# Kernel optimization log

Measured on AMD Instinct MI355X. Metric: run time of the kernel, lower is better.

The kernel has to match this reference:

```python
import jax, jax.numpy as jnp
import numpy as np

D = 768      # num_hiddens (hardcoded by dense1/dense2/ln in the source)
H = 12       # num_heads
NEG = -1000000.0
EPS = 1e-5


def setup_inputs() -> dict:
    key = jax.random.key(0)
    ks = jax.random.split(key, 14)
    B, Lq, Lk = 8, 1024, 1024
    s = 0.02
    return {
        "queries": jax.random.normal(ks[0], (B, Lq, D), dtype=jnp.float32),
        "keys":    jax.random.normal(ks[1], (B, Lk, D), dtype=jnp.float32),
        "values":  jax.random.normal(ks[2], (B, Lk, D), dtype=jnp.float32),
        # binary padding masks; count_nonzero along axis 1 gives valid lens
        "mask_1": jax.random.randint(ks[3], (B, Lk), 0, 2, dtype=jnp.int32),
        "mask_2": jax.random.randint(ks[4], (B, Lq), 0, 2, dtype=jnp.int32),
        # projection weights stored as [in, out] (torch Linear is y = x @ W.T)
        "Wq": jax.random.normal(ks[5], (D, D), dtype=jnp.float32) * s,
        "Wk": jax.random.normal(ks[6], (D, D), dtype=jnp.float32) * s,
        "Wv": jax.random.normal(ks[7], (D, D), dtype=jnp.float32) * s,
        "Wo": jax.random.normal(ks[8], (D, D), dtype=jnp.float32) * s,
        "d1_w": jax.random.normal(ks[9], (D, D), dtype=jnp.float32) * s,
        "d1_b": jnp.zeros((D,), dtype=jnp.float32),
        "d2_w": jax.random.normal(ks[10], (D, D), dtype=jnp.float32) * s,
        "d2_b": jnp.zeros((D,), dtype=jnp.float32),
        "ln_g": jnp.ones((D,), dtype=jnp.float32),
        "ln_b": jnp.zeros((D,), dtype=jnp.float32),
    }


def _cross_att(queries, keys, values, mask_1, mask_2,
               Wq, Wk, Wv, Wo, d1_w, d1_b, d2_w, d2_b, ln_g, ln_b):
    B, Lq, _ = queries.shape
    Lk = keys.shape[1]
    hd = D // H
    # project + split heads: [B, H, L, hd]
    q = (queries @ Wq).reshape(B, Lq, H, hd).transpose(0, 2, 1, 3)
    k = (keys    @ Wk).reshape(B, Lk, H, hd).transpose(0, 2, 1, 3)
    v = (values  @ Wv).reshape(B, Lk, H, hd).transpose(0, 2, 1, 3)
    scores = jnp.einsum('bhqd,bhkd->bhqk', q, k) / jnp.sqrt(jnp.float32(hd))
    # dual-axis prefix mask from nonzero counts
    vl1 = jnp.sum(mask_1 != 0, axis=1)  # [B], masks key axis
    vl2 = jnp.sum(mask_2 != 0, axis=1)  # [B], masks query axis
    col_ok = jnp.arange(Lk)[None, None, None, :] < vl1[:, None, None, None]
    row_ok = jnp.arange(Lq)[None, None, :, None] < vl2[:, None, None, None]
    scores = jnp.where(col_ok & row_ok, scores, NEG)
    attn = jax.nn.softmax(scores, axis=-1)
    out = jnp.einsum('bhqk,bhkd->bhqd', attn, v)
    out = out.transpose(0, 2, 1, 3).reshape(B, Lq, D)
    mha = out @ Wo
    ffn = jax.nn.relu(mha @ d1_w + d1_b) @ d2_w + d2_b
    x = ffn + mha  # dropout is identity in eval
    mu = jnp.mean(x, axis=-1, keepdims=True)
    var = jnp.mean(jnp.square(x - mu), axis=-1, keepdims=True)
    return (x - mu) / jnp.sqrt(var + EPS) * ln_g + ln_b


def reference(queries, keys, values, mask_1, mask_2,
              Wq, Wk, Wv, Wo, d1_w, d1_b, d2_w, d2_b, ln_g, ln_b):
    return _cross_att(queries, keys, values, mask_1, mask_2,
                      Wq, Wk, Wv, Wo, d1_w, d1_b, d2_w, d2_b, ln_g, ln_b)
```

## Files before the change

kernel.cpp:

```cpp
#include <hip/hip_runtime.h>
#include <hip/hip_bf16.h>
#include <type_traits>

#define DM   768
#define NH   12
#define HD   64
#define BATCH 8
#define SEQ  1024
#define NROWS (BATCH * SEQ)

typedef short bf16x8 __attribute__((ext_vector_type(8)));
typedef float f32x4 __attribute__((ext_vector_type(4)));

__device__ inline unsigned short f2b(float x) {
    union { float f; unsigned int u; } v; v.f = x;
    return (unsigned short)((v.u + 0x8000u) >> 16);
}
__device__ inline unsigned int f2b2(float lo, float hi) {
    union { float f; unsigned int u; } a, b; a.f = lo; b.f = hi;
    return __builtin_amdgcn_perm(b.u + 0x8000u, a.u + 0x8000u, 0x07060302u);
}
__device__ inline float b2f(unsigned short u) {
    union { float f; unsigned int x; } v; v.x = ((unsigned int)u) << 16;
    return v.f;
}

__device__ inline void gld16(const unsigned short* g, unsigned short* l) {
    __builtin_amdgcn_global_load_lds(
        (const __attribute__((address_space(1))) unsigned int*)g,
        (__attribute__((address_space(3))) unsigned int*)l, 16, 0, 0);
}

__global__ __launch_bounds__(256) void prep_kernel(const float* __restrict__ w0,
                                                   const float* __restrict__ w1,
                                                   const float* __restrict__ w2,
                                                   const float* __restrict__ w3,
                                                   const float* __restrict__ w4,
                                                   const float* __restrict__ w5,
                                                   unsigned short* __restrict__ wt,
                                                   const int* __restrict__ m1,
                                                   const int* __restrict__ m2,
                                                   int* __restrict__ lens,
                                                   const float* __restrict__ qin,
                                                   const float* __restrict__ kin,
                                                   const float* __restrict__ vin,
                                                   unsigned short* __restrict__ oq,
                                                   unsigned short* __restrict__ ok,
                                                   unsigned short* __restrict__ ov) {
    const int z = blockIdx.z;
    const int t = threadIdx.x;

    if (z >= 7) {
        const int linear = (z - 7) * 576 + blockIdx.y * 24 + blockIdx.x;
        const int g = linear / 3072;
        const int r = linear % 3072;
        const float* src = (g == 0) ? qin : (g == 1) ? kin : vin;
        unsigned short* dst = (g == 0) ? oq : (g == 1) ? ok : ov;
        const size_t i = ((size_t)r * 256 + t) * 8;
        float4 f0 = ((const float4*)(src + i))[0];
        float4 f1 = ((const float4*)(src + i))[1];
        uint4 p;
        p.x = f2b2(f0.x, f0.y); p.y = f2b2(f0.z, f0.w);
        p.z = f2b2(f1.x, f1.y); p.w = f2b2(f1.z, f1.w);
        *(uint4*)(dst + i) = p;
        return;
    }

    if (z < 6) {
        __shared__ float tile[32][33];
        const float* W = (z == 0) ? w0 : (z == 1) ? w1 : (z == 2) ? w2
                       : (z == 3) ? w3 : (z == 4) ? w4 : w5;
        unsigned short* Wt = wt + (size_t)z * DM * DM;
        const int n0 = blockIdx.x * 32;
        const int k0 = blockIdx.y * 32;
        const int tx = t & 31;
        const int ty = t >> 5;
#pragma unroll
        for (int r = 0; r < 4; ++r)
            tile[ty + 8 * r][tx] = W[(size_t)(k0 + ty + 8 * r) * DM + n0 + tx];
        __syncthreads();
#pragma unroll
        for (int r = 0; r < 4; ++r)
            Wt[(size_t)(n0 + ty + 8 * r) * DM + k0 + tx] = f2b(tile[tx][ty + 8 * r]);
        return;
    }

    if (blockIdx.y == 12) {
        if (blockIdx.x >= 16) return;
        __shared__ int redi[256];
        const int bid = blockIdx.x;
        const int b = bid & 7;
        const int* m = (bid < 8) ? m1 : m2;
        int cnt = 0;
        for (int i = t; i < SEQ; i += 256) cnt += (m[b * SEQ + i] != 0) ? 1 : 0;
        redi[t] = cnt;
        __syncthreads();
        for (int off = 128; off > 0; off >>= 1) {
            if (t < off) redi[t] += redi[t + off];
            __syncthreads();
        }
        if (t == 0) lens[bid] = redi[0];
        return;
    }

    if (blockIdx.x >= 12 || blockIdx.y >= 12) return;
    {
        __shared__ __align__(16) unsigned short As[64][40];
        __shared__ __align__(16) unsigned short Bs[64][40];
        unsigned short* out = wt + (size_t)6 * DM * DM;
        const float* Wo = w3;
        const float* d1w = w4;
        const int mb = blockIdx.x * 64;
        const int nb = blockIdx.y * 64;
        const int wid = t >> 6, lane = t & 63;
        const int quad = lane >> 4, l16 = lane & 15;
        const int bk = t >> 3, bn = (t & 7) * 8;
        const int am = t >> 2, ak = (t & 3) * 8;

        f32x4 acc[4];
#pragma unroll
        for (int c = 0; c < 4; ++c) acc[c] = (f32x4){0.f, 0.f, 0.f, 0.f};

        for (int j0 = 0; j0 < DM; j0 += 32) {
            {
                const float* s = &d1w[(size_t)(j0 + bk) * DM + mb + bn];
                float4 f0 = ((const float4*)s)[0];
                float4 f1 = ((const float4*)s)[1];
                As[bn + 0][bk] = f2b(f0.x); As[bn + 1][bk] = f2b(f0.y);
                As[bn + 2][bk] = f2b(f0.z); As[bn + 3][bk] = f2b(f0.w);
                As[bn + 4][bk] = f2b(f1.x); As[bn + 5][bk] = f2b(f1.y);
                As[bn + 6][bk] = f2b(f1.z); As[bn + 7][bk] = f2b(f1.w);
            }
            {
                const float* s = &Wo[(size_t)(nb + am) * DM + j0 + ak];
                float4 f0 = ((const float4*)s)[0];
                float4 f1 = ((const float4*)s)[1];
                uint4 p;
                p.x = f2b2(f0.x, f0.y); p.y = f2b2(f0.z, f0.w);
                p.z = f2b2(f1.x, f1.y); p.w = f2b2(f1.z, f1.w);
                *(uint4*)&Bs[am][ak] = p;
            }
            __syncthreads();
            bf16x8 av = *(const bf16x8*)&As[16 * wid + l16][quad * 8];
#pragma unroll
            for (int c = 0; c < 4; ++c) {
                bf16x8 bv = *(const bf16x8*)&Bs[16 * c + l16][quad * 8];
                acc[c] = __builtin_amdgcn_mfma_f32_16x16x32_bf16(av, bv, acc[c], 0, 0, 0);
            }
            __syncthreads();
        }
#pragma unroll
        for (int c = 0; c < 4; ++c) {
            const int col = nb + 16 * c + l16;
#pragma unroll
            for (int r = 0; r < 4; ++r) {
                const int row = mb + 16 * wid + quad * 4 + r;
                out[(size_t)row * DM + col] = f2b(acc[c][r]);
            }
        }
    }
}

__global__ __launch_bounds__(256) void qkv_gemm(const unsigned short* __restrict__ aq,
                                                const unsigned short* __restrict__ akk,
                                                const unsigned short* __restrict__ av_,
                                                const unsigned short* __restrict__ wt,
                                                unsigned short* __restrict__ c0,
                                                unsigned short* __restrict__ c1,
                                                unsigned short* __restrict__ c2) {
    __shared__ __align__(16) unsigned short As[128][32];
    __shared__ __align__(16) unsigned short Ws[128][32];

    const int t = threadIdx.x;
    const int g = blockIdx.y / 6;
    const int m0 = blockIdx.x * 128;
    const int n0 = (blockIdx.y % 6) * 128;
    const unsigned short* A = (g == 0) ? aq : (g == 1) ? akk : av_;
    const unsigned short* Wt = wt + (size_t)g * DM * DM;
    unsigned short* C = (g == 0) ? c0 : (g == 1) ? c1 : c2;
    const float cs = (g == 0) ? 0.18033688f : 1.0f;

    const int w = t >> 6, lane = t & 63;
    const int quad = lane >> 4, l16 = lane & 15;
    const int wm = w & 1, wn = w >> 1;
    const int srow = 16 * w + (lane >> 2);
    const int scol = 8 * ((lane & 3) ^ ((lane >> 3) & 3));
    const int swr = (quad ^ ((l16 >> 1) & 3)) * 8;

    f32x4 acc[4][4];
#pragma unroll
    for (int i = 0; i < 4; ++i)
#pragma unroll
        for (int j = 0; j < 4; ++j) acc[i][j] = (f32x4){0.f, 0.f, 0.f, 0.f};

    for (int k0 = 0; k0 < DM; k0 += 32) {
#pragma unroll
        for (int j = 0; j < 2; ++j) {
            gld16(&A[(size_t)(m0 + srow + 64 * j) * DM + k0 + scol],
                  &As[16 * w + 64 * j][0]);
            gld16(&Wt[(size_t)(n0 + srow + 64 * j) * DM + k0 + scol],
                  &Ws[16 * w + 64 * j][0]);
        }
        __syncthreads();

        bf16x8 av[4], bv[4];
#pragma unroll
        for (int i = 0; i < 4; ++i)
            av[i] = *(const bf16x8*)&As[wm * 64 + 16 * i + l16][swr];
#pragma unroll
        for (int i = 0; i < 4; ++i)
            bv[i] = *(const bf16x8*)&Ws[wn * 64 + 16 * i + l16][swr];
#pragma unroll
        for (int i = 0; i < 4; ++i)
#pragma unroll
            for (int j = 0; j < 4; ++j)
                acc[i][j] = __builtin_amdgcn_mfma_f32_16x16x32_bf16(av[i], bv[j], acc[i][j], 0, 0, 0);
        __syncthreads();
    }

#pragma unroll
    for (int i = 0; i < 4; ++i)
#pragma unroll
        for (int j = 0; j < 4; ++j) {
            const int gn = n0 + wn * 64 + 16 * j + l16;
#pragma unroll
            for (int r = 0; r < 4; ++r) {
                const int gm = m0 + wm * 64 + 16 * i + quad * 4 + r;
                C[(size_t)gm * DM + gn] = f2b(acc[i][j][r] * cs);
            }
        }
}

__global__ __launch_bounds__(256) void vpart_kernel(const unsigned short* __restrict__ v,
                                                    float* __restrict__ vp) {
    __shared__ float red[4][64];
    const int t = threadIdx.x;
    const int bh = blockIdx.x;
    const int chunk = blockIdx.y;
    const int b = bh / NH, h = bh % NH;
    const int d = t & 63, rg = t >> 6;
    const unsigned short* base =
        v + (size_t)(b * SEQ + chunk * 128 + rg * 32) * DM + h * HD + d;
    float s = 0.0f;
#pragma unroll 4
    for (int i = 0; i < 32; ++i) s += b2f(base[(size_t)i * DM]);
    red[rg][d] = s;
    __syncthreads();
    if (rg == 0)
        vp[((size_t)bh * 8 + chunk) * 64 + d] = red[0][d] + red[1][d] + red[2][d] + red[3][d];
}

template <typename CT>
__global__ __launch_bounds__(256) void gemm_bf(const unsigned short* __restrict__ A,
                                               const unsigned short* __restrict__ Wt,
                                               CT* __restrict__ C,
                                               const float* __restrict__ bias,
                                               const unsigned short* __restrict__ res,
                                               int relu) {
    __shared__ __align__(16) unsigned short As[128][32];
    __shared__ __align__(16) unsigned short Ws[128][32];

    const int t = threadIdx.x;
    const int m0 = blockIdx.x * 128;
    const int n0 = blockIdx.y * 128;
    const int w = t >> 6, lane = t & 63;
    const int quad = lane >> 4, l16 = lane & 15;
    const int wm = w & 1, wn = w >> 1;
    const int srow = 16 * w + (lane >> 2);
    const int scol = 8 * ((lane & 3) ^ ((lane >> 3) & 3));
    const int swr = (quad ^ ((l16 >> 1) & 3)) * 8;

    f32x4 acc[4][4];
#pragma unroll
    for (int i = 0; i < 4; ++i)
#pragma unroll
        for (int j = 0; j < 4; ++j) acc[i][j] = (f32x4){0.f, 0.f, 0.f, 0.f};

    for (int k0 = 0; k0 < DM; k0 += 32) {
#pragma unroll
        for (int j = 0; j < 2; ++j) {
            gld16(&A[(size_t)(m0 + srow + 64 * j) * DM + k0 + scol],
                  &As[16 * w + 64 * j][0]);
            gld16(&Wt[(size_t)(n0 + srow + 64 * j) * DM + k0 + scol],
                  &Ws[16 * w + 64 * j][0]);
        }
        __syncthreads();

        bf16x8 av[4], bv[4];
#pragma unroll
        for (int i = 0; i < 4; ++i)
            av[i] = *(const bf16x8*)&As[wm * 64 + 16 * i + l16][swr];
#pragma unroll
        for (int i = 0; i < 4; ++i)
            bv[i] = *(const bf16x8*)&Ws[wn * 64 + 16 * i + l16][swr];
#pragma unroll
        for (int i = 0; i < 4; ++i)
#pragma unroll
            for (int j = 0; j < 4; ++j)
                acc[i][j] = __builtin_amdgcn_mfma_f32_16x16x32_bf16(av[i], bv[j], acc[i][j], 0, 0, 0);
        __syncthreads();
    }

#pragma unroll
    for (int i = 0; i < 4; ++i)
#pragma unroll
        for (int j = 0; j < 4; ++j) {
            const int gn = n0 + wn * 64 + 16 * j + l16;
            const float badd = bias ? bias[gn] : 0.0f;
#pragma unroll
            for (int r = 0; r < 4; ++r) {
                const int gm = m0 + wm * 64 + 16 * i + quad * 4 + r;
                float cv = acc[i][j][r] + badd;
                if (relu) cv = fmaxf(cv, 0.0f);
                if (res) cv += b2f(res[(size_t)gm * DM + gn]);
                if constexpr (std::is_same<CT, float>::value) {
                    C[(size_t)gm * DM + gn] = cv;
                } else {
                    C[(size_t)gm * DM + gn] = f2b(cv);
                }
            }
        }
}

__global__ __launch_bounds__(256) void gemm_mh(const unsigned short* __restrict__ A,
                                               const unsigned short* __restrict__ wt,
                                               unsigned short* __restrict__ cm,
                                               unsigned short* __restrict__ ch,
                                               const float* __restrict__ d1b) {
    __shared__ __align__(16) unsigned short As[128][32];
    __shared__ __align__(16) unsigned short Ws[128][32];

    const int t = threadIdx.x;
    const int unit = blockIdx.y / 6;
    const unsigned short* Wt = wt + (size_t)(unit ? 6 : 3) * DM * DM;
    unsigned short* C = unit ? ch : cm;
    const int m0 = blockIdx.x * 128;
    const int n0 = (blockIdx.y % 6) * 128;
    const int w = t >> 6, lane = t & 63;
    const int quad = lane >> 4, l16 = lane & 15;
    const int wm = w & 1, wn = w >> 1;
    const int srow = 16 * w + (lane >> 2);
    const int scol = 8 * ((lane & 3) ^ ((lane >> 3) & 3));
    const int swr = (quad ^ ((l16 >> 1) & 3)) * 8;

    f32x4 acc[4][4];
#pragma unroll
    for (int i = 0; i < 4; ++i)
#pragma unroll
        for (int j = 0; j < 4; ++j) acc[i][j] = (f32x4){0.f, 0.f, 0.f, 0.f};

    for (int k0 = 0; k0 < DM; k0 += 32) {
#pragma unroll
        for (int j = 0; j < 2; ++j) {
            gld16(&A[(size_t)(m0 + srow + 64 * j) * DM + k0 + scol],
                  &As[16 * w + 64 * j][0]);
            gld16(&Wt[(size_t)(n0 + srow + 64 * j) * DM + k0 + scol],
                  &Ws[16 * w + 64 * j][0]);
        }
        __syncthreads();

        bf16x8 av[4], bv[4];
#pragma unroll
        for (int i = 0; i < 4; ++i)
            av[i] = *(const bf16x8*)&As[wm * 64 + 16 * i + l16][swr];
#pragma unroll
        for (int i = 0; i < 4; ++i)
            bv[i] = *(const bf16x8*)&Ws[wn * 64 + 16 * i + l16][swr];
#pragma unroll
        for (int i = 0; i < 4; ++i)
#pragma unroll
            for (int j = 0; j < 4; ++j)
                acc[i][j] = __builtin_amdgcn_mfma_f32_16x16x32_bf16(av[i], bv[j], acc[i][j], 0, 0, 0);
        __syncthreads();
    }

#pragma unroll
    for (int i = 0; i < 4; ++i)
#pragma unroll
        for (int j = 0; j < 4; ++j) {
            const int gn = n0 + wn * 64 + 16 * j + l16;
            const float badd = unit ? d1b[gn] : 0.0f;
#pragma unroll
            for (int r = 0; r < 4; ++r) {
                const int gm = m0 + wm * 64 + 16 * i + quad * 4 + r;
                float cv = acc[i][j][r] + badd;
                if (unit) cv = fmaxf(cv, 0.0f);
                C[(size_t)gm * DM + gn] = f2b(cv);
            }
        }
}

__global__ __launch_bounds__(256) void attn_mfma(const unsigned short* Q,
                                                 const unsigned short* __restrict__ K,
                                                 const unsigned short* __restrict__ V,
                                                 unsigned short* O,
                                                 const int* __restrict__ lens,
                                                 const float* __restrict__ vp) {
    __shared__ __align__(16) unsigned short Ks[64][72];
    __shared__ __align__(16) unsigned short Vt[64][72];
    __shared__ __align__(16) unsigned short Ps[4][16][72];

    const int t = threadIdx.x;
    const int bid = blockIdx.x;
    const int q0 = (bid & 15) * 64;
    const int h = (bid >> 4) % NH;
    const int b = bid / (16 * NH);
    const int vl1 = lens[b];
    const int vl2 = lens[8 + b];
    const int wid = t >> 6;
    const int lane = t & 63;
    const int quad = lane >> 4;
    const int l16 = lane & 15;
    const size_t vpb = (size_t)(b * NH + h) * 8 * 64;

    if (q0 >= vl2 || vl1 == 0) {
        float vm[4];
#pragma unroll
        for (int ct = 0; ct < 4; ++ct) {
            float s = 0.0f;
#pragma unroll
            for (int c = 0; c < 8; ++c) s += vp[vpb + (size_t)c * 64 + 16 * ct + l16];
            vm[ct] = s * (1.0f / 1024.0f);
        }
#pragma unroll
        for (int r = 0; r < 4; ++r) {
            const size_t row = (size_t)(b * SEQ + q0 + 16 * wid + quad * 4 + r);
#pragma unroll
            for (int ct = 0; ct < 4; ++ct)
                O[row * DM + h * HD + 16 * ct + l16] = f2b(vm[ct]);
        }
        return;
    }

    bf16x8 qa0, qa1;
    {
        const unsigned short* qp =
            &Q[(size_t)(b * SEQ + q0 + 16 * wid + l16) * DM + h * HD + quad * 8];
        qa0 = *(const bf16x8*)qp;
        qa1 = *(const bf16x8*)(qp + 32);
    }

    f32x4 o[4];
#pragma unroll
    for (int ct = 0; ct < 4; ++ct) o[ct] = (f32x4){0.f, 0.f, 0.f, 0.f};
    float suml[4];
    bool rbad[4];
#pragma unroll
    for (int r = 0; r < 4; ++r) {
        suml[r] = 0.0f;
        rbad[r] = (q0 + 16 * wid + quad * 4 + r) >= vl2;
    }

    const int nt = (vl1 + 63) >> 6;

    const int kkr = t >> 3;
    const int khc = (t & 7) * 8;
    const unsigned short* kbase = &K[(size_t)(b * SEQ) * DM + h * HD];
    const unsigned short* vbase = &V[(size_t)(b * SEQ) * DM + h * HD];

    uint4 kr0 = *(const uint4*)&kbase[(size_t)kkr * DM + khc];
    uint4 kr1 = *(const uint4*)&kbase[(size_t)(kkr + 32) * DM + khc];
    uint4 vr0 = *(const uint4*)&vbase[(size_t)lane * DM + wid * 16];
    uint4 vr1 = *(const uint4*)&vbase[(size_t)lane * DM + wid * 16 + 8];

    const int k2 = l16 >> 2;

    for (int tile = 0; tile < nt; ++tile) {
        const int c0 = tile * 64;
        *(uint4*)&Ks[kkr][khc] = kr0;
        *(uint4*)&Ks[kkr + 32][khc] = kr1;
        {
            union { uint4 u; unsigned short s[8]; } va, vb;
            va.u = vr0; vb.u = vr1;
#pragma unroll
            for (int j = 0; j < 8; ++j) Vt[wid * 16 + j][lane] = va.s[j];
#pragma unroll
            for (int j = 0; j < 8; ++j) Vt[wid * 16 + 8 + j][lane] = vb.s[j];
        }
        __syncthreads();

        if (tile < nt - 1) {
            const int c1 = c0 + 64;
            kr0 = *(const uint4*)&kbase[(size_t)(c1 + kkr) * DM + khc];
            kr1 = *(const uint4*)&kbase[(size_t)(c1 + kkr + 32) * DM + khc];
            vr0 = *(const uint4*)&vbase[(size_t)(c1 + lane) * DM + wid * 16];
            vr1 = *(const uint4*)&vbase[(size_t)(c1 + lane) * DM + wid * 16 + 8];
        }

        f32x4 s[4];
#pragma unroll
        for (int ct = 0; ct < 4; ++ct) {
            f32x4 acc = (f32x4){0.f, 0.f, 0.f, 0.f};
            bf16x8 b0v = *(const bf16x8*)&Ks[16 * ct + l16][quad * 8];
            bf16x8 b1v = *(const bf16x8*)&Ks[16 * ct + l16][32 + quad * 8];
            acc = __builtin_amdgcn_mfma_f32_16x16x32_bf16(qa0, b0v, acc, 0, 0, 0);
            acc = __builtin_amdgcn_mfma_f32_16x16x32_bf16(qa1, b1v, acc, 0, 0, 0);
            s[ct] = acc;
        }
#pragma unroll
        for (int ct = 0; ct < 4; ++ct) {
            const bool kok = (c0 + 16 * ct + l16) < vl1;
#pragma unroll
            for (int r = 0; r < 4; ++r) {
                float e = __builtin_amdgcn_exp2f(s[ct][r]);
                float p = kok ? e : 0.0f;
                s[ct][r] = p;
                suml[r] += p;
            }
        }
#pragma unroll
        for (int ct = 0; ct < 4; ++ct) {
            const int gidx = 2 * ct + (l16 >> 3);
            const int c = l16 & 7;
            const int gs = (gidx ^ quad) * 8 + c;
#pragma unroll
            for (int r = 0; r < 4; ++r)
                Ps[wid][quad * 4 + r][gs] = f2b(s[ct][r]);
        }
        bf16x8 pa0 = *(const bf16x8*)&Ps[wid][l16][(quad ^ k2) * 8];
        bf16x8 pa1 = *(const bf16x8*)&Ps[wid][l16][((4 + quad) ^ k2) * 8];
#pragma unroll
        for (int ct = 0; ct < 4; ++ct) {
            bf16x8 vb0 = *(const bf16x8*)&Vt[16 * ct + l16][quad * 8];
            bf16x8 vb1 = *(const bf16x8*)&Vt[16 * ct + l16][32 + quad * 8];
            o[ct] = __builtin_amdgcn_mfma_f32_16x16x32_bf16(pa0, vb0, o[ct], 0, 0, 0);
            o[ct] = __builtin_amdgcn_mfma_f32_16x16x32_bf16(pa1, vb1, o[ct], 0, 0, 0);
        }
        __syncthreads();
    }

#pragma unroll
    for (int d = 1; d < 16; d <<= 1) {
#pragma unroll
        for (int r = 0; r < 4; ++r) suml[r] += __shfl_xor(suml[r], d, 64);
    }

    float vm[4];
    if (rbad[0] || rbad[3]) {
#pragma unroll
        for (int ct = 0; ct < 4; ++ct) {
            float s = 0.0f;
#pragma unroll
            for (int c = 0; c < 8; ++c) s += vp[vpb + (size_t)c * 64 + 16 * ct + l16];
            vm[ct] = s * (1.0f / 1024.0f);
        }
    }
#pragma unroll
    for (int r = 0; r < 4; ++r) {
        const float inv = 1.0f / suml[r];
        const size_t row = (size_t)(b * SEQ + q0 + 16 * wid + quad * 4 + r);
#pragma unroll
        for (int ct = 0; ct < 4; ++ct) {
            const float val = rbad[r] ? vm[ct] : o[ct][r] * inv;
            O[row * DM + h * HD + 16 * ct + l16] = f2b(val);
        }
    }
}

__global__ __launch_bounds__(256) void ln_kernel(float* __restrict__ X,
                                                 const float* __restrict__ g,
                                                 const float* __restrict__ bvec) {
    __shared__ float red[256];
    const int row = blockIdx.x;
    const int t = threadIdx.x;
    float* xr = X + (size_t)row * DM;
    float x0 = xr[t];
    float x1 = xr[t + 256];
    float x2 = xr[t + 512];
    red[t] = x0 + x1 + x2;
    __syncthreads();
    for (int off = 128; off > 0; off >>= 1) {
        if (t < off) red[t] += red[t + off];
        __syncthreads();
    }
    float mu = red[0] * (1.0f / 768.0f);
    __syncthreads();
    float d0 = x0 - mu, d1 = x1 - mu, d2 = x2 - mu;
    red[t] = d0 * d0 + d1 * d1 + d2 * d2;
    __syncthreads();
    for (int off = 128; off > 0; off >>= 1) {
        if (t < off) red[t] += red[t + off];
        __syncthreads();
    }
    float rstd = rsqrtf(red[0] * (1.0f / 768.0f) + 1e-5f);
    xr[t]       = d0 * rstd * g[t]       + bvec[t];
    xr[t + 256] = d1 * rstd * g[t + 256] + bvec[t + 256];
    xr[t + 512] = d2 * rstd * g[t + 512] + bvec[t + 512];
}

extern "C" void kernel_launch(void* const* d_in, const int* in_sizes, int n_in,
                              void* d_out, int out_size, void* d_ws, size_t ws_size,
                              hipStream_t stream) {
    const float* queries = (const float*)d_in[0];
    const float* keys    = (const float*)d_in[1];
    const float* values  = (const float*)d_in[2];
    const int* mask1 = (const int*)d_in[3];
    const int* mask2 = (const int*)d_in[4];
    const float* Wq  = (const float*)d_in[5];
    const float* Wk  = (const float*)d_in[6];
    const float* Wv  = (const float*)d_in[7];
    const float* Wo  = (const float*)d_in[8];
    const float* d1w = (const float*)d_in[9];
    const float* d1b = (const float*)d_in[10];
    const float* d2w = (const float*)d_in[11];
    const float* d2b = (const float*)d_in[12];
    const float* lng = (const float*)d_in[13];
    const float* lnb = (const float*)d_in[14];

    char* ws = (char*)d_ws;
    int* lens = (int*)ws;
    float* vp = (float*)(ws + 256);
    const size_t VP = (size_t)96 * 8 * 64 * sizeof(float);
    const size_t NB = (size_t)NROWS * DM * sizeof(unsigned short);
    const size_t WT = (size_t)DM * DM;
    unsigned short* b0 = (unsigned short*)(ws + 256 + VP);
    unsigned short* b1 = (unsigned short*)(ws + 256 + VP + NB);
    unsigned short* b2 = (unsigned short*)(ws + 256 + VP + 2 * NB);
    unsigned short* wt = (unsigned short*)(ws + 256 + VP + 3 * NB);
    unsigned short* aq = (unsigned short*)(ws + 256 + VP + 3 * NB + 7 * WT * sizeof(unsigned short));
    unsigned short* ak = aq + (size_t)NROWS * DM;
    unsigned short* av = ak + (size_t)NROWS * DM;
    float* xout = (float*)d_out;

    prep_kernel<<<dim3(24, 24, 23), 256, 0, stream>>>(Wq, Wk, Wv, Wo, d1w, d2w,
                                                      wt, mask1, mask2, lens,
                                                      queries, keys, values,
                                                      aq, ak, av);

    qkv_gemm<<<dim3(64, 18), 256, 0, stream>>>(aq, ak, av, wt, b0, b1, b2);

    vpart_kernel<<<dim3(96, 8), 256, 0, stream>>>(b2, vp);

    attn_mfma<<<16 * NH * BATCH, 256, 0, stream>>>(b0, b1, b2, b0, lens, vp);

    gemm_mh<<<dim3(64, 12), 256, 0, stream>>>(b0, wt, b1, b2, d1b);

    gemm_bf<float><<<dim3(64, 6), 256, 0, stream>>>(b2, wt + 5 * WT, xout, d2b, b1, 0);

    ln_kernel<<<NROWS, 256, 0, stream>>>(xout, lng, lnb);
}
```

Before: 311.4 us.

## Move Wo·d1 weight fold and mask lengths into QKV GEMM grid; vectorize epilogue stores

Moves the small Wo×d1_w weight-product GEMM and the mask-length reduction out of the prep kernel and into extra blocks of the QKV GEMM launch. This shortens the prep kernel's serial critical path and lets that work overlap with the large projection GEMM. Separately, the GEMM epilogues swap the MFMA operand order so each lane holds four consecutive output columns, allowing packed 8-byte bf16 (or 16-byte float) stores and vector bias/residual loads instead of scalar scattered writes. The risk is that the QKV kernel's tail now includes 144 long serial-K blocks.

```diff
diff --git a/kernel.cpp b/kernel.cpp
--- a/kernel.cpp
+++ b/kernel.cpp
@@ -38,9 +38,6 @@
                                                    const float* __restrict__ w4,
                                                    const float* __restrict__ w5,
                                                    unsigned short* __restrict__ wt,
-                                                   const int* __restrict__ m1,
-                                                   const int* __restrict__ m2,
-                                                   int* __restrict__ lens,
                                                    const float* __restrict__ qin,
                                                    const float* __restrict__ kin,
                                                    const float* __restrict__ vin,
@@ -50,8 +47,8 @@
     const int z = blockIdx.z;
     const int t = threadIdx.x;
 
-    if (z >= 7) {
-        const int linear = (z - 7) * 576 + blockIdx.y * 24 + blockIdx.x;
+    if (z >= 6) {
+        const int linear = (z - 6) * 576 + blockIdx.y * 24 + blockIdx.x;
         const int g = linear / 3072;
         const int r = linear % 3072;
         const float* src = (g == 0) ? qin : (g == 1) ? kin : vin;
@@ -66,7 +63,7 @@
         return;
     }
 
-    if (z < 6) {
+    {
         __shared__ float tile[32][33];
         const float* W = (z == 0) ? w0 : (z == 1) ? w1 : (z == 2) ? w2
                        : (z == 3) ? w3 : (z == 4) ? w4 : w5;
@@ -82,96 +79,98 @@
 #pragma unroll
         for (int r = 0; r < 4; ++r)
             Wt[(size_t)(n0 + ty + 8 * r) * DM + k0 + tx] = f2b(tile[tx][ty + 8 * r]);
-        return;
-    }
-
-    if (blockIdx.y == 12) {
-        if (blockIdx.x >= 16) return;
-        __shared__ int redi[256];
-        const int bid = blockIdx.x;
-        const int b = bid & 7;
-        const int* m = (bid < 8) ? m1 : m2;
-        int cnt = 0;
-        for (int i = t; i < SEQ; i += 256) cnt += (m[b * SEQ + i] != 0) ? 1 : 0;
-        redi[t] = cnt;
-        __syncthreads();
-        for (int off = 128; off > 0; off >>= 1) {
-            if (t < off) redi[t] += redi[t + off];
-            __syncthreads();
-        }
-        if (t == 0) lens[bid] = redi[0];
-        return;
-    }
-
-    if (blockIdx.x >= 12 || blockIdx.y >= 12) return;
-    {
-        __shared__ __align__(16) unsigned short As[64][40];
-        __shared__ __align__(16) unsigned short Bs[64][40];
-        unsigned short* out = wt + (size_t)6 * DM * DM;
-        const float* Wo = w3;
-        const float* d1w = w4;
-        const int mb = blockIdx.x * 64;
-        const int nb = blockIdx.y * 64;
-        const int wid = t >> 6, lane = t & 63;
-        const int quad = lane >> 4, l16 = lane & 15;
-        const int bk = t >> 3, bn = (t & 7) * 8;
-        const int am = t >> 2, ak = (t & 3) * 8;
-
-        f32x4 acc[4];
-#pragma unroll
-        for (int c = 0; c < 4; ++c) acc[c] = (f32x4){0.f, 0.f, 0.f, 0.f};
-
-        for (int j0 = 0; j0 < DM; j0 += 32) {
-            {
-                const float* s = &d1w[(size_t)(j0 + bk) * DM + mb + bn];
-                float4 f0 = ((const float4*)s)[0];
-                float4 f1 = ((const float4*)s)[1];
-                As[bn + 0][bk] = f2b(f0.x); As[bn + 1][bk] = f2b(f0.y);
-                As[bn + 2][bk] = f2b(f0.z); As[bn + 3][bk] = f2b(f0.w);
-                As[bn + 4][bk] = f2b(f1.x); As[bn + 5][bk] = f2b(f1.y);
-                As[bn + 6][bk] = f2b(f1.z); As[bn + 7][bk] = f2b(f1.w);
-            }
-            {
-                const float* s = &Wo[(size_t)(nb + am) * DM + j0 + ak];
-                float4 f0 = ((const float4*)s)[0];
-                float4 f1 = ((const float4*)s)[1];
-                uint4 p;
-                p.x = f2b2(f0.x, f0.y); p.y = f2b2(f0.z, f0.w);
-                p.z = f2b2(f1.x, f1.y); p.w = f2b2(f1.z, f1.w);
-                *(uint4*)&Bs[am][ak] = p;
-            }
-            __syncthreads();
-            bf16x8 av = *(const bf16x8*)&As[16 * wid + l16][quad * 8];
-#pragma unroll
-            for (int c = 0; c < 4; ++c) {
-                bf16x8 bv = *(const bf16x8*)&Bs[16 * c + l16][quad * 8];
-                acc[c] = __builtin_amdgcn_mfma_f32_16x16x32_bf16(av, bv, acc[c], 0, 0, 0);
-            }
-            __syncthreads();
-        }
-#pragma unroll
-        for (int c = 0; c < 4; ++c) {
-            const int col = nb + 16 * c + l16;
-#pragma unroll
-            for (int r = 0; r < 4; ++r) {
-                const int row = mb + 16 * wid + quad * 4 + r;
-                out[(size_t)row * DM + col] = f2b(acc[c][r]);
-            }
-        }
     }
 }
 
 __global__ __launch_bounds__(256) void qkv_gemm(const unsigned short* __restrict__ aq,
                                                 const unsigned short* __restrict__ akk,
                                                 const unsigned short* __restrict__ av_,
-                                                const unsigned short* __restrict__ wt,
+                                                unsigned short* __restrict__ wt,
                                                 unsigned short* __restrict__ c0,
                                                 unsigned short* __restrict__ c1,
-                                                unsigned short* __restrict__ c2) {
+                                                unsigned short* __restrict__ c2,
+                                                const float* __restrict__ wof,
+                                                const float* __restrict__ d1wf,
+                                                const int* __restrict__ m1,
+                                                const int* __restrict__ m2,
+                                                int* __restrict__ lens) {
     __shared__ __align__(16) unsigned short As[128][32];
     __shared__ __align__(16) unsigned short Ws[128][32];
 
     const int t = threadIdx.x;
+
+    if (blockIdx.y >= 18) {
+        const int id = (blockIdx.y - 18) * 64 + blockIdx.x;
+        if (id < 144) {
+            unsigned short (*As40)[40] = (unsigned short(*)[40])&As[0][0];
+            unsigned short (*Bs40)[40] = (unsigned short(*)[40])&Ws[0][0];
+            unsigned short* out = wt + (size_t)6 * DM * DM;
+            const int mb = (id % 12) * 64;
+            const int nb = (id / 12) * 64;
+            const int wid = t >> 6, lane = t & 63;
+            const int quad = lane >> 4, l16 = lane & 15;
+            const int bk = t >> 3, bn = (t & 7) * 8;
+            const int am = t >> 2, ak = (t & 3) * 8;
+
+            f32x4 acc[4];
+#pragma unroll
+            for (int c = 0; c < 4; ++c) acc[c] = (f32x4){0.f, 0.f, 0.f, 0.f};
+
+            for (int j0 = 0; j0 < DM; j0 += 32) {
+                {
+                    const float* s = &d1wf[(size_t)(j0 + bk) * DM + mb + bn];
+                    float4 f0 = ((const float4*)s)[0];
+                    float4 f1 = ((const float4*)s)[1];
+                    As40[bn + 0][bk] = f2b(f0.x); As40[bn + 1][bk] = f2b(f0.y);
+                    As40[bn + 2][bk] = f2b(f0.z); As40[bn + 3][bk] = f2b(f0.w);
+                    As40[bn + 4][bk] = f2b(f1.x); As40[bn + 5][bk] = f2b(f1.y);
+                    As40[bn + 6][bk] = f2b(f1.z); As40[bn + 7][bk] = f2b(f1.w);
+                }
+                {
+                    const float* s = &wof[(size_t)(nb + am) * DM + j0 + ak];
+                    float4 f0 = ((const float4*)s)[0];
+                    float4 f1 = ((const float4*)s)[1];
+                    uint4 p;
+                    p.x = f2b2(f0.x, f0.y); p.y = f2b2(f0.z, f0.w);
+                    p.z = f2b2(f1.x, f1.y); p.w = f2b2(f1.z, f1.w);
+                    *(uint4*)&Bs40[am][ak] = p;
+                }
+                __syncthreads();
+                bf16x8 a2 = *(const bf16x8*)&As40[16 * wid + l16][quad * 8];
+#pragma unroll
+                for (int c = 0; c < 4; ++c) {
+                    bf16x8 b2v = *(const bf16x8*)&Bs40[16 * c + l16][quad * 8];
+                    acc[c] = __builtin_amdgcn_mfma_f32_16x16x32_bf16(a2, b2v, acc[c], 0, 0, 0);
+                }
+                __syncthreads();
+            }
+#pragma unroll
+            for (int c = 0; c < 4; ++c) {
+                const int col = nb + 16 * c + l16;
+#pragma unroll
+                for (int r = 0; r < 4; ++r) {
+                    const int row = mb + 16 * wid + quad * 4 + r;
+                    out[(size_t)row * DM + col] = f2b(acc[c][r]);
+                }
+            }
+        } else if (id < 160) {
+            const int bid = id - 144;
+            int* redi = (int*)&As[0][0];
+            const int b = bid & 7;
+            const int* m = (bid < 8) ? m1 : m2;
+            int cnt = 0;
+            for (int i = t; i < SEQ; i += 256) cnt += (m[b * SEQ + i] != 0) ? 1 : 0;
+            redi[t] = cnt;
+            __syncthreads();
+            for (int off = 128; off > 0; off >>= 1) {
+                if (t < off) redi[t] += redi[t + off];
+                __syncthreads();
+            }
+            if (t == 0) lens[bid] = redi[0];
+        }
+        return;
+    }
+
     const int g = blockIdx.y / 6;
     const int m0 = blockIdx.x * 128;
     const int n0 = (blockIdx.y % 6) * 128;
@@ -214,21 +213,22 @@
         for (int i = 0; i < 4; ++i)
 #pragma unroll
             for (int j = 0; j < 4; ++j)
-                acc[i][j] = __builtin_amdgcn_mfma_f32_16x16x32_bf16(av[i], bv[j], acc[i][j], 0, 0, 0);
-        __syncthreads();
-    }
-
-#pragma unroll
-    for (int i = 0; i < 4; ++i)
+                acc[i][j] = __builtin_amdgcn_mfma_f32_16x16x32_bf16(bv[j], av[i], acc[i][j], 0, 0, 0);
+        __syncthreads();
+    }
+
+#pragma unroll
+    for (int i = 0; i < 4; ++i) {
+        const int tok = m0 + wm * 64 + 16 * i + l16;
+        unsigned short* crow = &C[(size_t)tok * DM + n0 + wn * 64 + quad * 4];
 #pragma unroll
         for (int j = 0; j < 4; ++j) {
-            const int gn = n0 + wn * 64 + 16 * j + l16;
-#pragma unroll
-            for (int r = 0; r < 4; ++r) {
-                const int gm = m0 + wm * 64 + 16 * i + quad * 4 + r;
-                C[(size_t)gm * DM + gn] = f2b(acc[i][j][r] * cs);
-            }
-        }
+            uint2 pr;
+            pr.x = f2b2(acc[i][j][0] * cs, acc[i][j][1] * cs);
+            pr.y = f2b2(acc[i][j][2] * cs, acc[i][j][3] * cs);
+            *(uint2*)(crow + 16 * j) = pr;
+        }
+    }
 }
 
 __global__ __launch_bounds__(256) void vpart_kernel(const unsigned short* __restrict__ v,
@@ -297,29 +297,44 @@
         for (int i = 0; i < 4; ++i)
 #pragma unroll
             for (int j = 0; j < 4; ++j)
-                acc[i][j] = __builtin_amdgcn_mfma_f32_16x16x32_bf16(av[i], bv[j], acc[i][j], 0, 0, 0);
-        __syncthreads();
-    }
-
-#pragma unroll
-    for (int i = 0; i < 4; ++i)
+                acc[i][j] = __builtin_amdgcn_mfma_f32_16x16x32_bf16(bv[j], av[i], acc[i][j], 0, 0, 0);
+        __syncthreads();
+    }
+
+#pragma unroll
+    for (int i = 0; i < 4; ++i) {
+        const int tok = m0 + wm * 64 + 16 * i + l16;
 #pragma unroll
         for (int j = 0; j < 4; ++j) {
-            const int gn = n0 + wn * 64 + 16 * j + l16;
-            const float badd = bias ? bias[gn] : 0.0f;
-#pragma unroll
-            for (int r = 0; r < 4; ++r) {
-                const int gm = m0 + wm * 64 + 16 * i + quad * 4 + r;
-                float cv = acc[i][j][r] + badd;
-                if (relu) cv = fmaxf(cv, 0.0f);
-                if (res) cv += b2f(res[(size_t)gm * DM + gn]);
-                if constexpr (std::is_same<CT, float>::value) {
-                    C[(size_t)gm * DM + gn] = cv;
-                } else {
-                    C[(size_t)gm * DM + gn] = f2b(cv);
-                }
-            }
-        }
+            const int fb = n0 + wn * 64 + 16 * j + quad * 4;
+            float cv0 = acc[i][j][0], cv1 = acc[i][j][1];
+            float cv2 = acc[i][j][2], cv3 = acc[i][j][3];
+            if (bias) {
+                const float4 bb = *(const float4*)&bias[fb];
+                cv0 += bb.x; cv1 += bb.y; cv2 += bb.z; cv3 += bb.w;
+            }
+            if (relu) {
+                cv0 = fmaxf(cv0, 0.0f); cv1 = fmaxf(cv1, 0.0f);
+                cv2 = fmaxf(cv2, 0.0f); cv3 = fmaxf(cv3, 0.0f);
+            }
+            if (res) {
+                const uint2 rr = *(const uint2*)&res[(size_t)tok * DM + fb];
+                cv0 += b2f((unsigned short)(rr.x & 0xffffu));
+                cv1 += b2f((unsigned short)(rr.x >> 16));
+                cv2 += b2f((unsigned short)(rr.y & 0xffffu));
+                cv3 += b2f((unsigned short)(rr.y >> 16));
+            }
+            if constexpr (std::is_same<CT, float>::value) {
+                float4 o4; o4.x = cv0; o4.y = cv1; o4.z = cv2; o4.w = cv3;
+                *(float4*)&C[(size_t)tok * DM + fb] = o4;
+            } else {
+                uint2 pr;
+                pr.x = f2b2(cv0, cv1);
+                pr.y = f2b2(cv2, cv3);
+                *(uint2*)&C[(size_t)tok * DM + fb] = pr;
+            }
+        }
+    }
 }
 
 __global__ __launch_bounds__(256) void gemm_mh(const unsigned short* __restrict__ A,
@@ -370,24 +385,31 @@
         for (int i = 0; i < 4; ++i)
 #pragma unroll
             for (int j = 0; j < 4; ++j)
-                acc[i][j] = __builtin_amdgcn_mfma_f32_16x16x32_bf16(av[i], bv[j], acc[i][j], 0, 0, 0);
-        __syncthreads();
-    }
-
-#pragma unroll
-    for (int i = 0; i < 4; ++i)
+                acc[i][j] = __builtin_amdgcn_mfma_f32_16x16x32_bf16(bv[j], av[i], acc[i][j], 0, 0, 0);
+        __syncthreads();
+    }
+
+#pragma unroll
+    for (int i = 0; i < 4; ++i) {
+        const int tok = m0 + wm * 64 + 16 * i + l16;
 #pragma unroll
         for (int j = 0; j < 4; ++j) {
-            const int gn = n0 + wn * 64 + 16 * j + l16;
-            const float badd = unit ? d1b[gn] : 0.0f;
-#pragma unroll
-            for (int r = 0; r < 4; ++r) {
-                const int gm = m0 + wm * 64 + 16 * i + quad * 4 + r;
-                float cv = acc[i][j][r] + badd;
-                if (unit) cv = fmaxf(cv, 0.0f);
-                C[(size_t)gm * DM + gn] = f2b(cv);
-            }
-        }
+            const int fb = n0 + wn * 64 + 16 * j + quad * 4;
+            float cv0 = acc[i][j][0], cv1 = acc[i][j][1];
+            float cv2 = acc[i][j][2], cv3 = acc[i][j][3];
+            if (unit) {
+                const float4 bb = *(const float4*)&d1b[fb];
+                cv0 = fmaxf(cv0 + bb.x, 0.0f);
+                cv1 = fmaxf(cv1 + bb.y, 0.0f);
+                cv2 = fmaxf(cv2 + bb.z, 0.0f);
+                cv3 = fmaxf(cv3 + bb.w, 0.0f);
+            }
+            uint2 pr;
+            pr.x = f2b2(cv0, cv1);
+            pr.y = f2b2(cv2, cv3);
+            *(uint2*)&C[(size_t)tok * DM + fb] = pr;
+        }
+    }
 }
 
 __global__ __launch_bounds__(256) void attn_mfma(const unsigned short* Q,
@@ -622,12 +644,12 @@
     unsigned short* av = ak + (size_t)NROWS * DM;
     float* xout = (float*)d_out;
 
-    prep_kernel<<<dim3(24, 24, 23), 256, 0, stream>>>(Wq, Wk, Wv, Wo, d1w, d2w,
-                                                      wt, mask1, mask2, lens,
-                                                      queries, keys, values,
+    prep_kernel<<<dim3(24, 24, 22), 256, 0, stream>>>(Wq, Wk, Wv, Wo, d1w, d2w,
+                                                      wt, queries, keys, values,
                                                       aq, ak, av);
 
-    qkv_gemm<<<dim3(64, 18), 256, 0, stream>>>(aq, ak, av, wt, b0, b1, b2);
+    qkv_gemm<<<dim3(64, 21), 256, 0, stream>>>(aq, ak, av, wt, b0, b1, b2,
+                                               Wo, d1w, mask1, mask2, lens);
 
     vpart_kernel<<<dim3(96, 8), 256, 0, stream>>>(b2, vp);
 
```

Measured after the change: 316.0 us. No clear change (+1.5%).
